# Kernel tuning notes

Measured on AMD Instinct MI355X. Metric: run time of the kernel, lower is better.

The kernel has to match this reference:

```python
import jax, jax.numpy as jnp
import numpy as np

N = 50000      # nodes
E = 600000     # edges (before self-loops)
F_IN = 128     # input features
H = 128        # hidden width
C = 64         # classes
NEG_SLOPE = 0.2


def setup_inputs() -> dict:
    key = jax.random.key(0)
    ks = jax.random.split(key, 16)
    x = jax.random.normal(ks[0], (N, F_IN), dtype=jnp.float32)
    edge_index = jax.random.randint(ks[1], (2, E), 0, N, dtype=jnp.int32)
    dims = [(F_IN, H), (H, H), (H, C)]
    inp = {"x": x, "edge_index": edge_index}
    for l, (din, dout) in enumerate(dims):
        kw, ka, kb = jax.random.split(ks[2 + l], 3)
        scale = 1.0 / np.sqrt(din)
        inp[f"W{l}"] = jax.random.normal(kw, (din, dout), dtype=jnp.float32) * scale
        inp[f"a_src{l}"] = jax.random.normal(ka, (dout,), dtype=jnp.float32) * 0.1
        inp[f"a_dst{l}"] = jax.random.normal(kb, (dout,), dtype=jnp.float32) * 0.1
        inp[f"b{l}"] = jnp.zeros((dout,), dtype=jnp.float32)
    return inp


def gat_conv(x, src, dst, W, a_s, a_d, b):
    n = x.shape[0]
    h = x @ W                                   # [n, dout]
    alpha = jax.nn.leaky_relu((h @ a_s)[src] + (h @ a_d)[dst], NEG_SLOPE)  # [e]
    # segment softmax over destination-node neighborhoods
    m = jax.ops.segment_max(alpha, dst, num_segments=n)
    ex = jnp.exp(alpha - m[dst])
    denom = jax.ops.segment_sum(ex, dst, num_segments=n)
    coef = ex / denom[dst]                      # [e]
    out = jax.ops.segment_sum(h[src] * coef[:, None], dst, num_segments=n)
    return out + b


def reference(x, edge_index, W0, a_src0, a_dst0, b0, W1, a_src1, a_dst1, b1, W2, a_src2, a_dst2, b2):
    n = x.shape[0]
    loops = jnp.arange(n, dtype=edge_index.dtype)   # add_self_loops=True (PyG default)
    src = jnp.concatenate([edge_index[0], loops])
    dst = jnp.concatenate([edge_index[1], loops])
    h = gat_conv(x, src, dst, W0, a_src0, a_dst0, b0)
    h = h * jax.nn.sigmoid(h)                        # SiLU between layers
    h = gat_conv(h, src, dst, W1, a_src1, a_dst1, b1)
    h = h * jax.nn.sigmoid(h)
    h = gat_conv(h, src, dst, W2, a_src2, a_dst2, b2)
    return jax.nn.log_softmax(h, axis=1)
```

## Files before the change

### kernel.cpp

```cpp
#include <hip/hip_runtime.h>
#include <math.h>

#define NEG_SLOPE 0.2f
constexpr int BS_SCAN = 1024;

typedef __attribute__((ext_vector_type(8))) short bfrag;
typedef __attribute__((ext_vector_type(4))) float f32x4;

__device__ __forceinline__ float lrelu(float x) { return x > 0.f ? x : NEG_SLOPE * x; }

__device__ __forceinline__ unsigned short f2bf(float f) {
    union { float f; unsigned u; } v; v.f = f;
    unsigned r = v.u + 0x7fffu + ((v.u >> 16) & 1u);
    return (unsigned short)(r >> 16);
}
__device__ __forceinline__ float bf2f_lo(unsigned p) { union { unsigned u; float f; } v; v.u = p << 16; return v.f; }
__device__ __forceinline__ float bf2f_hi(unsigned p) { union { unsigned u; float f; } v; v.u = p & 0xffff0000u; return v.f; }

__device__ __forceinline__ void wswz_body(const float* __restrict__ W, unsigned short* __restrict__ out,
                                          int DOUT, int tid) {
    int lane = tid & 63;
    int g = tid >> 6;
    int NT = DOUT >> 4;
    int tile = g % NT, kstep = g / NT;
    int q = lane >> 4, c = lane & 15;
    int n_ = tile * 16 + c;
    unsigned short v[8];
#pragma unroll
    for (int j = 0; j < 8; ++j) {
        int k = kstep * 32 + q * 8 + j;
        v[j] = f2bf(W[k * DOUT + n_]);
    }
    uint4 o;
    o.x = (unsigned)v[0] | ((unsigned)v[1] << 16);
    o.y = (unsigned)v[2] | ((unsigned)v[3] << 16);
    o.z = (unsigned)v[4] | ((unsigned)v[5] << 16);
    o.w = (unsigned)v[6] | ((unsigned)v[7] << 16);
    *(uint4*)(out + (size_t)tid * 8) = o;
}

__global__ __launch_bounds__(256) void swz_kernel(
    const float* __restrict__ W0, const float* __restrict__ W1, const float* __restrict__ W2,
    unsigned short* __restrict__ wz0, unsigned short* __restrict__ wz1, unsigned short* __restrict__ wz2)
{
    int wb = blockIdx.x;
    if (wb < 8)       wswz_body(W0, wz0, 128, wb * 256 + threadIdx.x);
    else if (wb < 16) wswz_body(W1, wz1, 128, (wb - 8) * 256 + threadIdx.x);
    else {
        int tid = (wb - 16) * 256 + threadIdx.x;
        if (tid < 1024) wswz_body(W2, wz2, 64, tid);
    }
}

__global__ __launch_bounds__(1024) void scan1_kernel(const int* __restrict__ counts,
                                                     int* __restrict__ excl,
                                                     int* __restrict__ totals, int n) {
    __shared__ int sm[BS_SCAN];
    int tid = threadIdx.x;
    int i = blockIdx.x * BS_SCAN + tid;
    int v = (i < n) ? counts[i] : 0;
    int val = v;
    sm[tid] = val;
    for (int off = 1; off < BS_SCAN; off <<= 1) {
        __syncthreads();
        int t = (tid >= off) ? sm[tid - off] : 0;
        __syncthreads();
        val += t; sm[tid] = val;
    }
    if (i < n) excl[i] = val - v;
    if (tid == BS_SCAN - 1) totals[blockIdx.x] = val;
}

__global__ __launch_bounds__(1024) void scan23_kernel(int* __restrict__ row_ptr,
                                                      const int* __restrict__ totals,
                                                      int n, int E, int nb) {
    __shared__ int s_off;
    int tid = threadIdx.x;
    if (tid < 64) {
        int v = (tid < blockIdx.x && tid < nb) ? totals[tid] : 0;
#pragma unroll
        for (int off = 32; off; off >>= 1) v += __shfl_xor(v, off);
        if (tid == 0) s_off = v;
    }
    __syncthreads();
    int off = s_off;
    int i = blockIdx.x * BS_SCAN + tid;
    if (i < n) row_ptr[i] += off;
    if (i == 0) row_ptr[n] = E;
}

template<int DOUT, bool ABF>
__device__ __forceinline__ void gemm_body(
    int bid, const void* __restrict__ Xv, const unsigned short* __restrict__ Wswz,
    const float* __restrict__ avs, const float* __restrict__ avd,
    unsigned* __restrict__ Hout, float* __restrict__ as_out, float* __restrict__ ad_out,
    int n, float* __restrict__ smemw)
{
    constexpr int NT = DOUT / 16;
    constexpr int NCH = NT / 4;
    int lane = threadIdx.x & 63;
    int w = threadIdx.x >> 6;
    int q = lane >> 4, c = lane & 15;
    int rowbase = bid * 64 + w * 16;
    int arow = rowbase + c;

    f32x4 acc[NT];
#pragma unroll
    for (int t = 0; t < NT; ++t) acc[t] = (f32x4){0.f, 0.f, 0.f, 0.f};

#pragma unroll
    for (int ks = 0; ks < 4; ++ks) {
        bfrag a = (bfrag)0;
        int k0 = ks * 32 + q * 8;
        if (ABF) {
            if (arow < n) a = *(const bfrag*)((const unsigned short*)Xv + (size_t)arow * 128 + k0);
        } else {
            if (arow < n) {
                const float* xp = (const float*)Xv + (size_t)arow * 128 + k0;
                float4 x0 = *(const float4*)xp, x1 = *(const float4*)(xp + 4);
                a[0] = (short)f2bf(x0.x); a[1] = (short)f2bf(x0.y);
                a[2] = (short)f2bf(x0.z); a[3] = (short)f2bf(x0.w);
                a[4] = (short)f2bf(x1.x); a[5] = (short)f2bf(x1.y);
                a[6] = (short)f2bf(x1.z); a[7] = (short)f2bf(x1.w);
            }
        }
#pragma unroll
        for (int t = 0; t < NT; ++t) {
            bfrag b = *(const bfrag*)(Wswz + ((size_t)(ks * NT + t) * 64 + lane) * 8);
            acc[t] = __builtin_amdgcn_mfma_f32_16x16x32_bf16(a, b, acc[t], 0, 0, 0);
        }
    }

    float* sm = smemw + w * (16 * 68);
    int dr = lane >> 2;
    int c0 = (lane & 3) * 16;
    float s = 0.f, d = 0.f;

#pragma unroll
    for (int ch = 0; ch < NCH; ++ch) {
        if (ch) {
            asm volatile("s_waitcnt lgkmcnt(0)" ::: "memory");
            __builtin_amdgcn_wave_barrier();
        }
#pragma unroll
        for (int t = 0; t < 4; ++t)
#pragma unroll
            for (int r = 0; r < 4; ++r)
                sm[(q * 4 + r) * 68 + t * 16 + c] = acc[ch * 4 + t][r];
        __builtin_amdgcn_wave_barrier();

#pragma unroll
        for (int it = 0; it < 4; ++it) {
            int r = it * 4 + q;
            int grow = rowbase + r;
            float4 v = *(const float4*)(sm + r * 68 + c * 4);
            uint2 o;
            o.x = (unsigned)f2bf(v.x) | ((unsigned)f2bf(v.y) << 16);
            o.y = (unsigned)f2bf(v.z) | ((unsigned)f2bf(v.w) << 16);
            if (grow < n) *(uint2*)(Hout + (size_t)grow * (DOUT / 2) + ch * 32 + c * 2) = o;
        }
#pragma unroll
        for (int j = 0; j < 16; j += 4) {
            float4 hv = *(const float4*)(sm + dr * 68 + c0 + j);
            float4 av = *(const float4*)(avs + ch * 64 + c0 + j);
            float4 dv = *(const float4*)(avd + ch * 64 + c0 + j);
            s += hv.x * av.x + hv.y * av.y + hv.z * av.z + hv.w * av.w;
            d += hv.x * dv.x + hv.y * dv.y + hv.z * dv.z + hv.w * dv.w;
        }
    }

    s += __shfl_down(s, 2); s += __shfl_down(s, 1);
    d += __shfl_down(d, 2); d += __shfl_down(d, 1);
    int grow = rowbase + dr;
    if ((lane & 3) == 0 && grow < n) { as_out[grow] = s; ad_out[grow] = d; }
}

__global__ __launch_bounds__(256) void fused0_kernel(
    const int* __restrict__ dstv, int* __restrict__ counts, int* __restrict__ rank, int E, int cb,
    const float* __restrict__ X, const unsigned short* __restrict__ wz0,
    const float* __restrict__ avs, const float* __restrict__ avd,
    unsigned* __restrict__ Hout, float* __restrict__ as_out, float* __restrict__ ad_out, int n)
{
    __shared__ float smem[4 * 16 * 68];
    int b = blockIdx.x;
    if (b < cb) {
        int blockbase = b * 4096 + (int)threadIdx.x * 4;
#pragma unroll
        for (int j = 0; j < 4; ++j) {
            int e0 = blockbase + j * 1024;
            if (e0 + 3 < E) {
                int4 d4 = *(const int4*)(dstv + e0);
                int4 r4;
                r4.x = atomicAdd(&counts[d4.x], 1);
                r4.y = atomicAdd(&counts[d4.y], 1);
                r4.z = atomicAdd(&counts[d4.z], 1);
                r4.w = atomicAdd(&counts[d4.w], 1);
                *(int4*)(rank + e0) = r4;
            } else {
#pragma unroll
                for (int k = 0; k < 4; ++k) {
                    int e = e0 + k;
                    if (e < E) rank[e] = atomicAdd(&counts[dstv[e]], 1);
                }
            }
        }
        return;
    }
    gemm_body<128, false>(b - cb, X, wz0, avs, avd, Hout, as_out, ad_out, n, smem);
}

template<int DOUT>
__global__ __launch_bounds__(256) void gemm_kernel(
    const unsigned* __restrict__ Xb, const unsigned short* __restrict__ Wswz,
    const float* __restrict__ avs, const float* __restrict__ avd,
    unsigned* __restrict__ Hout, float* __restrict__ as_out, float* __restrict__ ad_out, int n)
{
    __shared__ float smem[4 * 16 * 68];
    gemm_body<DOUT, true>(blockIdx.x, Xb, Wswz, avs, avd, Hout, as_out, ad_out, n, smem);
}

__global__ __launch_bounds__(256) void scatter_kernel(
    const int* __restrict__ ei, const int* __restrict__ rank,
    const int* __restrict__ row_ptr, unsigned short* __restrict__ col, int E)
{
    int blockbase = blockIdx.x * 2048 + (int)threadIdx.x * 4;
#pragma unroll
    for (int j = 0; j < 2; ++j) {
        int e0 = blockbase + j * 1024;
        if (e0 + 3 < E) {
            int4 s4 = *(const int4*)(ei + e0);
            int4 d4 = *(const int4*)(ei + E + e0);
            int4 r4 = *(const int4*)(rank + e0);
            col[row_ptr[d4.x] + r4.x] = (unsigned short)s4.x;
            col[row_ptr[d4.y] + r4.y] = (unsigned short)s4.y;
            col[row_ptr[d4.z] + r4.z] = (unsigned short)s4.z;
            col[row_ptr[d4.w] + r4.w] = (unsigned short)s4.w;
        } else {
#pragma unroll
            for (int k = 0; k < 4; ++k) {
                int e = e0 + k;
                if (e < E) col[row_ptr[ei[E + e]] + rank[e]] = (unsigned short)ei[e];
            }
        }
    }
}

__global__ __launch_bounds__(256) void agg128_kernel(
    const unsigned* __restrict__ Hb, const float* __restrict__ as_v,
    const float* __restrict__ ad_v, const float* __restrict__ bias,
    const int* __restrict__ row_ptr, const unsigned short* __restrict__ col,
    unsigned* __restrict__ outb, int n)
{
    int lane = threadIdx.x & 63;
    int node = blockIdx.x * 4 + (threadIdx.x >> 6);
    if (node >= n) return;
    int g = lane >> 4, i = lane & 15;
    int beg = row_ptr[node], end = row_ptr[node + 1];
    float adv = ad_v[node];
    float c_self = __expf(fminf(lrelu(as_v[node] + adv), 60.f));

    uint4 hs = *(const uint4*)(Hb + (size_t)node * 64 + i * 4);
    float cs0 = (g == 0) ? c_self : 0.f;
    float acc[8];
    acc[0] = cs0 * bf2f_lo(hs.x); acc[1] = cs0 * bf2f_hi(hs.x);
    acc[2] = cs0 * bf2f_lo(hs.y); acc[3] = cs0 * bf2f_hi(hs.y);
    acc[4] = cs0 * bf2f_lo(hs.z); acc[5] = cs0 * bf2f_hi(hs.z);
    acc[6] = cs0 * bf2f_lo(hs.w); acc[7] = cs0 * bf2f_hi(hs.w);
    float dsum = (lane == 0) ? c_self : 0.f;

    for (int cb = beg; cb < end; cb += 64) {
        int idx = cb + lane;
        int sreg = 0; float creg = 0.f;
        if (idx < end) {
            sreg = col[idx];
            creg = __expf(fminf(lrelu(as_v[sreg] + adv), 60.f));
        }
        dsum += creg;
        int cnt = end - cb; if (cnt > 64) cnt = 64;
        for (int k = 0; k < cnt; k += 8) {
            int kk0 = k + g, kk1 = k + g + 4;
            int s0 = __shfl(sreg, kk0);
            int s1 = __shfl(sreg, kk1);
            float c0 = __shfl(creg, kk0);
            float c1 = __shfl(creg, kk1);
            uint4 h0 = *(const uint4*)(Hb + (size_t)s0 * 64 + i * 4);
            uint4 h1 = *(const uint4*)(Hb + (size_t)s1 * 64 + i * 4);
            acc[0] += c0 * bf2f_lo(h0.x); acc[1] += c0 * bf2f_hi(h0.x);
            acc[2] += c0 * bf2f_lo(h0.y); acc[3] += c0 * bf2f_hi(h0.y);
            acc[4] += c0 * bf2f_lo(h0.z); acc[5] += c0 * bf2f_hi(h0.z);
            acc[6] += c0 * bf2f_lo(h0.w); acc[7] += c0 * bf2f_hi(h0.w);
            acc[0] += c1 * bf2f_lo(h1.x); acc[1] += c1 * bf2f_hi(h1.x);
            acc[2] += c1 * bf2f_lo(h1.y); acc[3] += c1 * bf2f_hi(h1.y);
            acc[4] += c1 * bf2f_lo(h1.z); acc[5] += c1 * bf2f_hi(h1.z);
            acc[6] += c1 * bf2f_lo(h1.w); acc[7] += c1 * bf2f_hi(h1.w);
        }
    }

#pragma unroll
    for (int off = 32; off; off >>= 1) dsum += __shfl_xor(dsum, off);
    float inv = 1.f / dsum;
#pragma unroll
    for (int j = 0; j < 8; ++j) { acc[j] += __shfl_xor(acc[j], 16); acc[j] += __shfl_xor(acc[j], 32); }

    if (g == 0) {
        float4 b0v = *(const float4*)(bias + i * 8);
        float4 b1v = *(const float4*)(bias + i * 8 + 4);
        float v0 = acc[0] * inv + b0v.x, v1 = acc[1] * inv + b0v.y;
        float v2 = acc[2] * inv + b0v.z, v3 = acc[3] * inv + b0v.w;
        float v4 = acc[4] * inv + b1v.x, v5 = acc[5] * inv + b1v.y;
        float v6 = acc[6] * inv + b1v.z, v7 = acc[7] * inv + b1v.w;
        v0 /= (1.f + __expf(-v0)); v1 /= (1.f + __expf(-v1));
        v2 /= (1.f + __expf(-v2)); v3 /= (1.f + __expf(-v3));
        v4 /= (1.f + __expf(-v4)); v5 /= (1.f + __expf(-v5));
        v6 /= (1.f + __expf(-v6)); v7 /= (1.f + __expf(-v7));
        uint4 o;
        o.x = (unsigned)f2bf(v0) | ((unsigned)f2bf(v1) << 16);
        o.y = (unsigned)f2bf(v2) | ((unsigned)f2bf(v3) << 16);
        o.z = (unsigned)f2bf(v4) | ((unsigned)f2bf(v5) << 16);
        o.w = (unsigned)f2bf(v6) | ((unsigned)f2bf(v7) << 16);
        *(uint4*)(outb + (size_t)node * 64 + i * 4) = o;
    }
}

__global__ __launch_bounds__(256) void agg64_kernel(
    const unsigned* __restrict__ Hb, const float* __restrict__ as_v,
    const float* __restrict__ ad_v, const float* __restrict__ bias,
    const int* __restrict__ row_ptr, const unsigned short* __restrict__ col,
    float* __restrict__ out, int n)
{
    int lane = threadIdx.x & 63;
    int node = blockIdx.x * 4 + (threadIdx.x >> 6);
    if (node >= n) return;
    int g = lane >> 4, i = lane & 15;
    int beg = row_ptr[node], end = row_ptr[node + 1];
    float adv = ad_v[node];
    float c_self = __expf(fminf(lrelu(as_v[node] + adv), 60.f));

    uint2 hs = *(const uint2*)(Hb + (size_t)node * 32 + i * 2);
    float cs0 = (g == 0) ? c_self : 0.f;
    float acc[4];
    acc[0] = cs0 * bf2f_lo(hs.x); acc[1] = cs0 * bf2f_hi(hs.x);
    acc[2] = cs0 * bf2f_lo(hs.y); acc[3] = cs0 * bf2f_hi(hs.y);
    float dsum = (lane == 0) ? c_self : 0.f;

    for (int cb = beg; cb < end; cb += 64) {
        int idx = cb + lane;
        int sreg = 0; float creg = 0.f;
        if (idx < end) {
            sreg = col[idx];
            creg = __expf(fminf(lrelu(as_v[sreg] + adv), 60.f));
        }
        dsum += creg;
        int cnt = end - cb; if (cnt > 64) cnt = 64;
        for (int k = 0; k < cnt; k += 8) {
            int kk0 = k + g, kk1 = k + g + 4;
            int s0 = __shfl(sreg, kk0);
            int s1 = __shfl(sreg, kk1);
            float c0 = __shfl(creg, kk0);
            float c1 = __shfl(creg, kk1);
            uint2 h0 = *(const uint2*)(Hb + (size_t)s0 * 32 + i * 2);
            uint2 h1 = *(const uint2*)(Hb + (size_t)s1 * 32 + i * 2);
            acc[0] += c0 * bf2f_lo(h0.x); acc[1] += c0 * bf2f_hi(h0.x);
            acc[2] += c0 * bf2f_lo(h0.y); acc[3] += c0 * bf2f_hi(h0.y);
            acc[0] += c1 * bf2f_lo(h1.x); acc[1] += c1 * bf2f_hi(h1.x);
            acc[2] += c1 * bf2f_lo(h1.y); acc[3] += c1 * bf2f_hi(h1.y);
        }
    }

#pragma unroll
    for (int off = 32; off; off >>= 1) dsum += __shfl_xor(dsum, off);
    float inv = 1.f / dsum;
#pragma unroll
    for (int j = 0; j < 4; ++j) { acc[j] += __shfl_xor(acc[j], 16); acc[j] += __shfl_xor(acc[j], 32); }

    float4 bv = *(const float4*)(bias + i * 4);
    float v0 = acc[0] * inv + bv.x, v1 = acc[1] * inv + bv.y;
    float v2 = acc[2] * inv + bv.z, v3 = acc[3] * inv + bv.w;
    float mx = fmaxf(fmaxf(v0, v1), fmaxf(v2, v3));
#pragma unroll
    for (int off = 8; off; off >>= 1) mx = fmaxf(mx, __shfl_xor(mx, off));
    float sum = __expf(v0 - mx) + __expf(v1 - mx) + __expf(v2 - mx) + __expf(v3 - mx);
#pragma unroll
    for (int off = 8; off; off >>= 1) sum += __shfl_xor(sum, off);
    float ls = mx + logf(sum);
    if (g == 0) {
        float4 o = make_float4(v0 - ls, v1 - ls, v2 - ls, v3 - ls);
        *(float4*)(out + (size_t)node * 64 + i * 4) = o;
    }
}

extern "C" void kernel_launch(void* const* d_in, const int* in_sizes, int n_in,
                              void* d_out, int out_size, void* d_ws, size_t ws_size,
                              hipStream_t stream) {
    const float* x   = (const float*)d_in[0];
    const int*   ei  = (const int*)d_in[1];
    const float* W0  = (const float*)d_in[2];
    const float* as0 = (const float*)d_in[3];
    const float* ad0 = (const float*)d_in[4];
    const float* b0  = (const float*)d_in[5];
    const float* W1  = (const float*)d_in[6];
    const float* as1 = (const float*)d_in[7];
    const float* ad1 = (const float*)d_in[8];
    const float* b1  = (const float*)d_in[9];
    const float* W2  = (const float*)d_in[10];
    const float* as2 = (const float*)d_in[11];
    const float* ad2 = (const float*)d_in[12];
    const float* b2  = (const float*)d_in[13];

    int n = in_sizes[0] / 128;
    int E = in_sizes[1] / 2;
    const int* dstv = ei + E;

    char* wsp = (char*)d_ws;
    auto alloc = [&](size_t bytes) {
        char* p = wsp;
        wsp += (bytes + 255) & ~(size_t)255;
        return p;
    };
    int*   counts  = (int*)alloc((size_t)n * 4);
    int*   row_ptr = (int*)alloc((size_t)(n + 1) * 4);
    int*   rank    = (int*)alloc((size_t)E * 4);
    int*   totals  = (int*)alloc(256 * 4);
    unsigned short* col = (unsigned short*)alloc((size_t)E * 2);
    unsigned short* wz0 = (unsigned short*)alloc(128 * 128 * 2);
    unsigned short* wz1 = (unsigned short*)alloc(128 * 128 * 2);
    unsigned short* wz2 = (unsigned short*)alloc(128 * 64 * 2);
    unsigned* hb0  = (unsigned*)alloc((size_t)n * 64 * 4);
    unsigned* hb1  = (unsigned*)alloc((size_t)n * 64 * 4);
    unsigned* hf   = (unsigned*)alloc((size_t)n * 32 * 4);
    unsigned* xb   = (unsigned*)alloc((size_t)n * 64 * 4);
    float*    asbA = (float*)alloc((size_t)n * 4);
    float*    adbA = (float*)alloc((size_t)n * 4);
    float*    asbB = (float*)alloc((size_t)n * 4);
    float*    adbB = (float*)alloc((size_t)n * 4);

    (void)hipMemsetAsync(counts, 0, (size_t)n * 4, stream);
    int cbc   = (E + 4095) / 4096;
    int cbs   = (E + 2047) / 2048;
    int gemmb = (n + 63) / 64;
    int nodeb = (n + 3) / 4;
    int nb = (n + BS_SCAN - 1) / BS_SCAN;

    swz_kernel<<<20, 256, 0, stream>>>(W0, W1, W2, wz0, wz1, wz2);
    fused0_kernel<<<cbc + gemmb, 256, 0, stream>>>(dstv, counts, rank, E, cbc,
                                                   x, wz0, as0, ad0, hb0, asbA, adbA, n);
    scan1_kernel<<<nb, BS_SCAN, 0, stream>>>(counts, row_ptr, totals, n);
    scan23_kernel<<<nb, BS_SCAN, 0, stream>>>(row_ptr, totals, n, E, nb);
    scatter_kernel<<<cbs, 256, 0, stream>>>(ei, rank, row_ptr, col, E);
    agg128_kernel<<<nodeb, 256, 0, stream>>>(hb0, asbA, adbA, b0, row_ptr, col, xb, n);
    gemm_kernel<128><<<gemmb, 256, 0, stream>>>(xb, wz1, as1, ad1, hb1, asbB, adbB, n);
    agg128_kernel<<<nodeb, 256, 0, stream>>>(hb1, asbB, adbB, b1, row_ptr, col, xb, n);
    gemm_kernel<64><<<gemmb, 256, 0, stream>>>(xb, wz2, as2, ad2, hf, asbA, adbA, n);
    agg64_kernel<<<nodeb, 256, 0, stream>>>(hf, asbA, adbA, b2, row_ptr, col, (float*)d_out, n);
}
```

Measured before the change: 261.8 us.

## Build CSR with cursor atomics instead of per-edge rank, fold memset, unroll gathers

The counting pass no longer stores a per-edge rank array. Instead the scan writes a per-node cursor, and the scatter kernel claims slots with atomicAdd on that cursor, batching 16 edges per thread. The counts memset is folded into the weight-swizzle kernel, which removes one launch. The aggregation inner loops now gather four neighbor rows per iteration instead of two, for more memory-level parallelism. Neighbor order within each CSR row becomes nondeterministic, which can change float summation order slightly, and the scatter now pays for atomics.

```diff
diff --git a/kernel.cpp b/kernel.cpp
--- a/kernel.cpp
+++ b/kernel.cpp
@@ -41,14 +41,18 @@
 
 __global__ __launch_bounds__(256) void swz_kernel(
     const float* __restrict__ W0, const float* __restrict__ W1, const float* __restrict__ W2,
-    unsigned short* __restrict__ wz0, unsigned short* __restrict__ wz1, unsigned short* __restrict__ wz2)
+    unsigned short* __restrict__ wz0, unsigned short* __restrict__ wz1, unsigned short* __restrict__ wz2,
+    int* __restrict__ counts, int n)
 {
     int wb = blockIdx.x;
     if (wb < 8)       wswz_body(W0, wz0, 128, wb * 256 + threadIdx.x);
     else if (wb < 16) wswz_body(W1, wz1, 128, (wb - 8) * 256 + threadIdx.x);
-    else {
+    else if (wb < 20) {
         int tid = (wb - 16) * 256 + threadIdx.x;
         if (tid < 1024) wswz_body(W2, wz2, 64, tid);
+    } else {
+        int i = (wb - 20) * 256 + (int)threadIdx.x;
+        if (i < n) counts[i] = 0;
     }
 }
 
@@ -73,7 +77,7 @@
 
 __global__ __launch_bounds__(1024) void scan23_kernel(int* __restrict__ row_ptr,
                                                       const int* __restrict__ totals,
-                                                      int n, int E, int nb) {
+                                                      int* __restrict__ cursor, int n, int E, int nb) {
     __shared__ int s_off;
     int tid = threadIdx.x;
     if (tid < 64) {
@@ -85,7 +89,11 @@
     __syncthreads();
     int off = s_off;
     int i = blockIdx.x * BS_SCAN + tid;
-    if (i < n) row_ptr[i] += off;
+    if (i < n) {
+        int rp = row_ptr[i] + off;
+        row_ptr[i] = rp;
+        cursor[i] = rp;
+    }
     if (i == 0) row_ptr[n] = E;
 }
 
@@ -176,7 +184,7 @@
 }
 
 __global__ __launch_bounds__(256) void fused0_kernel(
-    const int* __restrict__ dstv, int* __restrict__ counts, int* __restrict__ rank, int E, int cb,
+    const int* __restrict__ dstv, int* __restrict__ counts, int E, int cb,
     const float* __restrict__ X, const unsigned short* __restrict__ wz0,
     const float* __restrict__ avs, const float* __restrict__ avd,
     unsigned* __restrict__ Hout, float* __restrict__ as_out, float* __restrict__ ad_out, int n)
@@ -188,19 +196,17 @@
 #pragma unroll
         for (int j = 0; j < 4; ++j) {
             int e0 = blockbase + j * 1024;
-            if (e0 + 3 < E) {
+            if (((E & 3) == 0) && e0 + 3 < E) {
                 int4 d4 = *(const int4*)(dstv + e0);
-                int4 r4;
-                r4.x = atomicAdd(&counts[d4.x], 1);
-                r4.y = atomicAdd(&counts[d4.y], 1);
-                r4.z = atomicAdd(&counts[d4.z], 1);
-                r4.w = atomicAdd(&counts[d4.w], 1);
-                *(int4*)(rank + e0) = r4;
+                atomicAdd(&counts[d4.x], 1);
+                atomicAdd(&counts[d4.y], 1);
+                atomicAdd(&counts[d4.z], 1);
+                atomicAdd(&counts[d4.w], 1);
             } else {
 #pragma unroll
                 for (int k = 0; k < 4; ++k) {
                     int e = e0 + k;
-                    if (e < E) rank[e] = atomicAdd(&counts[dstv[e]], 1);
+                    if (e < E) atomicAdd(&counts[dstv[e]], 1);
                 }
             }
         }
@@ -220,26 +226,35 @@
 }
 
 __global__ __launch_bounds__(256) void scatter_kernel(
-    const int* __restrict__ ei, const int* __restrict__ rank,
-    const int* __restrict__ row_ptr, unsigned short* __restrict__ col, int E)
-{
-    int blockbase = blockIdx.x * 2048 + (int)threadIdx.x * 4;
-#pragma unroll
-    for (int j = 0; j < 2; ++j) {
-        int e0 = blockbase + j * 1024;
-        if (e0 + 3 < E) {
+    const int* __restrict__ ei, int* __restrict__ cursor,
+    unsigned short* __restrict__ col, int E)
+{
+    int blockbase = blockIdx.x * 4096 + (int)threadIdx.x * 4;
+    if (((E & 3) == 0) && (blockIdx.x + 1) * 4096 <= E) {
+        int dd[16], ss[16], pp[16];
+#pragma unroll
+        for (int j = 0; j < 4; ++j) {
+            int e0 = blockbase + j * 1024;
+            int4 d4 = *(const int4*)(ei + E + e0);
             int4 s4 = *(const int4*)(ei + e0);
-            int4 d4 = *(const int4*)(ei + E + e0);
-            int4 r4 = *(const int4*)(rank + e0);
-            col[row_ptr[d4.x] + r4.x] = (unsigned short)s4.x;
-            col[row_ptr[d4.y] + r4.y] = (unsigned short)s4.y;
-            col[row_ptr[d4.z] + r4.z] = (unsigned short)s4.z;
-            col[row_ptr[d4.w] + r4.w] = (unsigned short)s4.w;
-        } else {
+            dd[j * 4 + 0] = d4.x; dd[j * 4 + 1] = d4.y; dd[j * 4 + 2] = d4.z; dd[j * 4 + 3] = d4.w;
+            ss[j * 4 + 0] = s4.x; ss[j * 4 + 1] = s4.y; ss[j * 4 + 2] = s4.z; ss[j * 4 + 3] = s4.w;
+        }
+#pragma unroll
+        for (int i = 0; i < 16; ++i) pp[i] = atomicAdd(&cursor[dd[i]], 1);
+#pragma unroll
+        for (int i = 0; i < 16; ++i) col[pp[i]] = (unsigned short)ss[i];
+    } else {
+#pragma unroll
+        for (int j = 0; j < 4; ++j) {
+            int e0 = blockbase + j * 1024;
 #pragma unroll
             for (int k = 0; k < 4; ++k) {
                 int e = e0 + k;
-                if (e < E) col[row_ptr[ei[E + e]] + rank[e]] = (unsigned short)ei[e];
+                if (e < E) {
+                    int pos = atomicAdd(&cursor[ei[E + e]], 1);
+                    col[pos] = (unsigned short)ei[e];
+                }
             }
         }
     }
@@ -277,14 +292,20 @@
         }
         dsum += creg;
         int cnt = end - cb; if (cnt > 64) cnt = 64;
-        for (int k = 0; k < cnt; k += 8) {
-            int kk0 = k + g, kk1 = k + g + 4;
+        for (int k = 0; k < cnt; k += 16) {
+            int kk0 = k + g, kk1 = k + g + 4, kk2 = k + g + 8, kk3 = k + g + 12;
             int s0 = __shfl(sreg, kk0);
             int s1 = __shfl(sreg, kk1);
+            int s2 = __shfl(sreg, kk2);
+            int s3 = __shfl(sreg, kk3);
             float c0 = __shfl(creg, kk0);
             float c1 = __shfl(creg, kk1);
+            float c2 = __shfl(creg, kk2);
+            float c3 = __shfl(creg, kk3);
             uint4 h0 = *(const uint4*)(Hb + (size_t)s0 * 64 + i * 4);
             uint4 h1 = *(const uint4*)(Hb + (size_t)s1 * 64 + i * 4);
+            uint4 h2 = *(const uint4*)(Hb + (size_t)s2 * 64 + i * 4);
+            uint4 h3 = *(const uint4*)(Hb + (size_t)s3 * 64 + i * 4);
             acc[0] += c0 * bf2f_lo(h0.x); acc[1] += c0 * bf2f_hi(h0.x);
             acc[2] += c0 * bf2f_lo(h0.y); acc[3] += c0 * bf2f_hi(h0.y);
             acc[4] += c0 * bf2f_lo(h0.z); acc[5] += c0 * bf2f_hi(h0.z);
@@ -293,6 +314,14 @@
             acc[2] += c1 * bf2f_lo(h1.y); acc[3] += c1 * bf2f_hi(h1.y);
             acc[4] += c1 * bf2f_lo(h1.z); acc[5] += c1 * bf2f_hi(h1.z);
             acc[6] += c1 * bf2f_lo(h1.w); acc[7] += c1 * bf2f_hi(h1.w);
+            acc[0] += c2 * bf2f_lo(h2.x); acc[1] += c2 * bf2f_hi(h2.x);
+            acc[2] += c2 * bf2f_lo(h2.y); acc[3] += c2 * bf2f_hi(h2.y);
+            acc[4] += c2 * bf2f_lo(h2.z); acc[5] += c2 * bf2f_hi(h2.z);
+            acc[6] += c2 * bf2f_lo(h2.w); acc[7] += c2 * bf2f_hi(h2.w);
+            acc[0] += c3 * bf2f_lo(h3.x); acc[1] += c3 * bf2f_hi(h3.x);
+            acc[2] += c3 * bf2f_lo(h3.y); acc[3] += c3 * bf2f_hi(h3.y);
+            acc[4] += c3 * bf2f_lo(h3.z); acc[5] += c3 * bf2f_hi(h3.z);
+            acc[6] += c3 * bf2f_lo(h3.w); acc[7] += c3 * bf2f_hi(h3.w);
         }
     }
 
@@ -352,18 +381,28 @@
         }
         dsum += creg;
         int cnt = end - cb; if (cnt > 64) cnt = 64;
-        for (int k = 0; k < cnt; k += 8) {
-            int kk0 = k + g, kk1 = k + g + 4;
+        for (int k = 0; k < cnt; k += 16) {
+            int kk0 = k + g, kk1 = k + g + 4, kk2 = k + g + 8, kk3 = k + g + 12;
             int s0 = __shfl(sreg, kk0);
             int s1 = __shfl(sreg, kk1);
+            int s2 = __shfl(sreg, kk2);
+            int s3 = __shfl(sreg, kk3);
             float c0 = __shfl(creg, kk0);
             float c1 = __shfl(creg, kk1);
+            float c2 = __shfl(creg, kk2);
+            float c3 = __shfl(creg, kk3);
             uint2 h0 = *(const uint2*)(Hb + (size_t)s0 * 32 + i * 2);
             uint2 h1 = *(const uint2*)(Hb + (size_t)s1 * 32 + i * 2);
+            uint2 h2 = *(const uint2*)(Hb + (size_t)s2 * 32 + i * 2);
+            uint2 h3 = *(const uint2*)(Hb + (size_t)s3 * 32 + i * 2);
             acc[0] += c0 * bf2f_lo(h0.x); acc[1] += c0 * bf2f_hi(h0.x);
             acc[2] += c0 * bf2f_lo(h0.y); acc[3] += c0 * bf2f_hi(h0.y);
             acc[0] += c1 * bf2f_lo(h1.x); acc[1] += c1 * bf2f_hi(h1.x);
             acc[2] += c1 * bf2f_lo(h1.y); acc[3] += c1 * bf2f_hi(h1.y);
+            acc[0] += c2 * bf2f_lo(h2.x); acc[1] += c2 * bf2f_hi(h2.x);
+            acc[2] += c2 * bf2f_lo(h2.y); acc[3] += c2 * bf2f_hi(h2.y);
+            acc[0] += c3 * bf2f_lo(h3.x); acc[1] += c3 * bf2f_hi(h3.x);
+            acc[2] += c3 * bf2f_lo(h3.y); acc[3] += c3 * bf2f_hi(h3.y);
         }
     }
 
@@ -419,7 +458,7 @@
     };
     int*   counts  = (int*)alloc((size_t)n * 4);
     int*   row_ptr = (int*)alloc((size_t)(n + 1) * 4);
-    int*   rank    = (int*)alloc((size_t)E * 4);
+    int*   cursor  = (int*)alloc((size_t)n * 4);
     int*   totals  = (int*)alloc(256 * 4);
     unsigned short* col = (unsigned short*)alloc((size_t)E * 2);
     unsigned short* wz0 = (unsigned short*)alloc(128 * 128 * 2);
@@ -434,19 +473,18 @@
     float*    asbB = (float*)alloc((size_t)n * 4);
     float*    adbB = (float*)alloc((size_t)n * 4);
 
-    (void)hipMemsetAsync(counts, 0, (size_t)n * 4, stream);
     int cbc   = (E + 4095) / 4096;
-    int cbs   = (E + 2047) / 2048;
     int gemmb = (n + 63) / 64;
     int nodeb = (n + 3) / 4;
     int nb = (n + BS_SCAN - 1) / BS_SCAN;
-
-    swz_kernel<<<20, 256, 0, stream>>>(W0, W1, W2, wz0, wz1, wz2);
-    fused0_kernel<<<cbc + gemmb, 256, 0, stream>>>(dstv, counts, rank, E, cbc,
+    int zb = (n + 255) / 256;
+
+    swz_kernel<<<20 + zb, 256, 0, stream>>>(W0, W1, W2, wz0, wz1, wz2, counts, n);
+    fused0_kernel<<<cbc + gemmb, 256, 0, stream>>>(dstv, counts, E, cbc,
                                                    x, wz0, as0, ad0, hb0, asbA, adbA, n);
     scan1_kernel<<<nb, BS_SCAN, 0, stream>>>(counts, row_ptr, totals, n);
-    scan23_kernel<<<nb, BS_SCAN, 0, stream>>>(row_ptr, totals, n, E, nb);
-    scatter_kernel<<<cbs, 256, 0, stream>>>(ei, rank, row_ptr, col, E);
+    scan23_kernel<<<nb, BS_SCAN, 0, stream>>>(row_ptr, totals, cursor, n, E, nb);
+    scatter_kernel<<<cbc, 256, 0, stream>>>(ei, cursor, col, E);
     agg128_kernel<<<nodeb, 256, 0, stream>>>(hb0, asbA, adbA, b0, row_ptr, col, xb, n);
     gemm_kernel<128><<<gemmb, 256, 0, stream>>>(xb, wz1, as1, ad1, hb1, asbB, adbB, n);
     agg128_kernel<<<nodeb, 256, 0, stream>>>(hb1, asbB, adbB, b1, row_ptr, col, xb, n);
```

Result: slower. 273.8 us (+4.6%).

## Replace global atomic degree counting with per-block LDS byte histograms

Applied to the files above, without the earlier changes.

Edge-to-destination counting moves from global atomics into per-block shared-memory histograms of 8-bit counters packed four per word. Each block writes its histogram out, a new column-scan kernel forms per-block offsets and per-node counts, and the scatter kernel rebuilds each edge's slot from the block offset plus its local byte rank. Ranks shrink from int to byte. The cost is two large per-block histogram arrays, a serial scan over blocks, and a much larger shared-memory allocation that the fused GEMM blocks also carry. The packed byte counters assume every node's in-degree stays below 256, which holds only for low-degree graphs.

```diff
diff --git a/kernel.cpp b/kernel.cpp
--- a/kernel.cpp
+++ b/kernel.cpp
@@ -176,37 +176,104 @@
 }
 
 __global__ __launch_bounds__(256) void fused0_kernel(
-    const int* __restrict__ dstv, int* __restrict__ counts, int* __restrict__ rank, int E, int cb,
+    const int* __restrict__ dstv, unsigned* __restrict__ hist32, unsigned char* __restrict__ rank8,
+    int E, int hb, int nw,
     const float* __restrict__ X, const unsigned short* __restrict__ wz0,
     const float* __restrict__ avs, const float* __restrict__ avd,
     unsigned* __restrict__ Hout, float* __restrict__ as_out, float* __restrict__ ad_out, int n)
 {
-    __shared__ float smem[4 * 16 * 68];
+    __shared__ unsigned sbuf[12544];
     int b = blockIdx.x;
-    if (b < cb) {
-        int blockbase = b * 4096 + (int)threadIdx.x * 4;
+    if (b < hb) {
+        int tid = threadIdx.x;
+        for (int i = tid; i < nw; i += 256) sbuf[i] = 0u;
+        __syncthreads();
+        int base = b * 4096;
 #pragma unroll
         for (int j = 0; j < 4; ++j) {
-            int e0 = blockbase + j * 1024;
+            int e0 = base + j * 1024 + tid * 4;
             if (e0 + 3 < E) {
                 int4 d4 = *(const int4*)(dstv + e0);
-                int4 r4;
-                r4.x = atomicAdd(&counts[d4.x], 1);
-                r4.y = atomicAdd(&counts[d4.y], 1);
-                r4.z = atomicAdd(&counts[d4.z], 1);
-                r4.w = atomicAdd(&counts[d4.w], 1);
-                *(int4*)(rank + e0) = r4;
+                unsigned r0, r1, r2, r3;
+                { int sh = (d4.x & 3) * 8; r0 = (atomicAdd(&sbuf[d4.x >> 2], 1u << sh) >> sh) & 0xffu; }
+                { int sh = (d4.y & 3) * 8; r1 = (atomicAdd(&sbuf[d4.y >> 2], 1u << sh) >> sh) & 0xffu; }
+                { int sh = (d4.z & 3) * 8; r2 = (atomicAdd(&sbuf[d4.z >> 2], 1u << sh) >> sh) & 0xffu; }
+                { int sh = (d4.w & 3) * 8; r3 = (atomicAdd(&sbuf[d4.w >> 2], 1u << sh) >> sh) & 0xffu; }
+                *(unsigned*)(rank8 + e0) = r0 | (r1 << 8) | (r2 << 16) | (r3 << 24);
             } else {
-#pragma unroll
                 for (int k = 0; k < 4; ++k) {
                     int e = e0 + k;
-                    if (e < E) rank[e] = atomicAdd(&counts[dstv[e]], 1);
+                    if (e < E) {
+                        int d = dstv[e];
+                        int sh = (d & 3) * 8;
+                        rank8[e] = (unsigned char)((atomicAdd(&sbuf[d >> 2], 1u << sh) >> sh) & 0xffu);
+                    }
                 }
             }
         }
+        __syncthreads();
+        unsigned* hrow = hist32 + (size_t)b * nw;
+        for (int i = tid; i < nw; i += 256) hrow[i] = sbuf[i];
         return;
     }
-    gemm_body<128, false>(b - cb, X, wz0, avs, avd, Hout, as_out, ad_out, n, smem);
+    gemm_body<128, false>(b - hb, X, wz0, avs, avd, Hout, as_out, ad_out, n, (float*)sbuf);
+}
+
+__global__ __launch_bounds__(256) void colscan_kernel(
+    const unsigned* __restrict__ hist32, unsigned* __restrict__ off32,
+    int* __restrict__ counts, int hb, int nw, int n)
+{
+    int iw = blockIdx.x * 256 + (int)threadIdx.x;
+    if (iw >= nw) return;
+    unsigned run = 0;
+    for (int b = 0; b < hb; ++b) {
+        size_t idx = (size_t)b * nw + iw;
+        unsigned c = hist32[idx];
+        off32[idx] = run;
+        run += c;
+    }
+    int i0 = iw * 4;
+    int4 cv;
+    cv.x = (int)(run & 0xffu); cv.y = (int)((run >> 8) & 0xffu);
+    cv.z = (int)((run >> 16) & 0xffu); cv.w = (int)((run >> 24) & 0xffu);
+    if (i0 + 3 < n) *(int4*)(counts + i0) = cv;
+    else {
+        if (i0 < n)     counts[i0] = cv.x;
+        if (i0 + 1 < n) counts[i0 + 1] = cv.y;
+        if (i0 + 2 < n) counts[i0 + 2] = cv.z;
+        if (i0 + 3 < n) counts[i0 + 3] = cv.w;
+    }
+}
+
+__global__ __launch_bounds__(256) void scatter_kernel(
+    const int* __restrict__ ei, const unsigned char* __restrict__ rank8,
+    const unsigned* __restrict__ off32, const int* __restrict__ row_ptr,
+    unsigned short* __restrict__ col, int E, int nw)
+{
+    int e0 = (blockIdx.x * 256 + (int)threadIdx.x) * 4;
+    if (e0 + 3 < E) {
+        int4 s4 = *(const int4*)(ei + e0);
+        int4 d4 = *(const int4*)(ei + E + e0);
+        unsigned r4 = *(const unsigned*)(rank8 + e0);
+        size_t bb = (size_t)(e0 >> 12) * nw;
+        unsigned o0 = (off32[bb + (d4.x >> 2)] >> ((d4.x & 3) * 8)) & 0xffu;
+        unsigned o1 = (off32[bb + (d4.y >> 2)] >> ((d4.y & 3) * 8)) & 0xffu;
+        unsigned o2 = (off32[bb + (d4.z >> 2)] >> ((d4.z & 3) * 8)) & 0xffu;
+        unsigned o3 = (off32[bb + (d4.w >> 2)] >> ((d4.w & 3) * 8)) & 0xffu;
+        col[row_ptr[d4.x] + (int)o0 + (int)(r4 & 0xffu)]         = (unsigned short)s4.x;
+        col[row_ptr[d4.y] + (int)o1 + (int)((r4 >> 8) & 0xffu)]  = (unsigned short)s4.y;
+        col[row_ptr[d4.z] + (int)o2 + (int)((r4 >> 16) & 0xffu)] = (unsigned short)s4.z;
+        col[row_ptr[d4.w] + (int)o3 + (int)((r4 >> 24) & 0xffu)] = (unsigned short)s4.w;
+    } else {
+        for (int k = 0; k < 4; ++k) {
+            int e = e0 + k;
+            if (e < E) {
+                int d = ei[E + e];
+                unsigned o = (off32[(size_t)(e >> 12) * nw + (d >> 2)] >> ((d & 3) * 8)) & 0xffu;
+                col[row_ptr[d] + (int)o + (int)rank8[e]] = (unsigned short)ei[e];
+            }
+        }
+    }
 }
 
 template<int DOUT>
@@ -217,32 +284,6 @@
 {
     __shared__ float smem[4 * 16 * 68];
     gemm_body<DOUT, true>(blockIdx.x, Xb, Wswz, avs, avd, Hout, as_out, ad_out, n, smem);
-}
-
-__global__ __launch_bounds__(256) void scatter_kernel(
-    const int* __restrict__ ei, const int* __restrict__ rank,
-    const int* __restrict__ row_ptr, unsigned short* __restrict__ col, int E)
-{
-    int blockbase = blockIdx.x * 2048 + (int)threadIdx.x * 4;
-#pragma unroll
-    for (int j = 0; j < 2; ++j) {
-        int e0 = blockbase + j * 1024;
-        if (e0 + 3 < E) {
-            int4 s4 = *(const int4*)(ei + e0);
-            int4 d4 = *(const int4*)(ei + E + e0);
-            int4 r4 = *(const int4*)(rank + e0);
-            col[row_ptr[d4.x] + r4.x] = (unsigned short)s4.x;
-            col[row_ptr[d4.y] + r4.y] = (unsigned short)s4.y;
-            col[row_ptr[d4.z] + r4.z] = (unsigned short)s4.z;
-            col[row_ptr[d4.w] + r4.w] = (unsigned short)s4.w;
-        } else {
-#pragma unroll
-            for (int k = 0; k < 4; ++k) {
-                int e = e0 + k;
-                if (e < E) col[row_ptr[ei[E + e]] + rank[e]] = (unsigned short)ei[e];
-            }
-        }
-    }
 }
 
 __global__ __launch_bounds__(256) void agg128_kernel(
@@ -411,6 +452,9 @@
     int E = in_sizes[1] / 2;
     const int* dstv = ei + E;
 
+    int hb = (E + 4095) >> 12;
+    int nw = (n + 3) >> 2;
+
     char* wsp = (char*)d_ws;
     auto alloc = [&](size_t bytes) {
         char* p = wsp;
@@ -419,8 +463,10 @@
     };
     int*   counts  = (int*)alloc((size_t)n * 4);
     int*   row_ptr = (int*)alloc((size_t)(n + 1) * 4);
-    int*   rank    = (int*)alloc((size_t)E * 4);
     int*   totals  = (int*)alloc(256 * 4);
+    unsigned* hist32 = (unsigned*)alloc((size_t)hb * nw * 4);
+    unsigned* off32  = (unsigned*)alloc((size_t)hb * nw * 4);
+    unsigned char* rank8 = (unsigned char*)alloc((size_t)E);
     unsigned short* col = (unsigned short*)alloc((size_t)E * 2);
     unsigned short* wz0 = (unsigned short*)alloc(128 * 128 * 2);
     unsigned short* wz1 = (unsigned short*)alloc(128 * 128 * 2);
@@ -434,19 +480,19 @@
     float*    asbB = (float*)alloc((size_t)n * 4);
     float*    adbB = (float*)alloc((size_t)n * 4);
 
-    (void)hipMemsetAsync(counts, 0, (size_t)n * 4, stream);
-    int cbc   = (E + 4095) / 4096;
-    int cbs   = (E + 2047) / 2048;
     int gemmb = (n + 63) / 64;
     int nodeb = (n + 3) / 4;
-    int nb = (n + BS_SCAN - 1) / BS_SCAN;
+    int nb  = (n + BS_SCAN - 1) / BS_SCAN;
+    int cwb = (nw + 255) / 256;
+    int scb = (E + 1023) / 1024;
 
     swz_kernel<<<20, 256, 0, stream>>>(W0, W1, W2, wz0, wz1, wz2);
-    fused0_kernel<<<cbc + gemmb, 256, 0, stream>>>(dstv, counts, rank, E, cbc,
-                                                   x, wz0, as0, ad0, hb0, asbA, adbA, n);
+    fused0_kernel<<<hb + gemmb, 256, 0, stream>>>(dstv, hist32, rank8, E, hb, nw,
+                                                  x, wz0, as0, ad0, hb0, asbA, adbA, n);
+    colscan_kernel<<<cwb, 256, 0, stream>>>(hist32, off32, counts, hb, nw, n);
     scan1_kernel<<<nb, BS_SCAN, 0, stream>>>(counts, row_ptr, totals, n);
     scan23_kernel<<<nb, BS_SCAN, 0, stream>>>(row_ptr, totals, n, E, nb);
-    scatter_kernel<<<cbs, 256, 0, stream>>>(ei, rank, row_ptr, col, E);
+    scatter_kernel<<<scb, 256, 0, stream>>>(ei, rank8, off32, row_ptr, col, E, nw);
     agg128_kernel<<<nodeb, 256, 0, stream>>>(hb0, asbA, adbA, b0, row_ptr, col, xb, n);
     gemm_kernel<128><<<gemmb, 256, 0, stream>>>(xb, wz1, as1, ad1, hb1, asbB, adbB, n);
     agg128_kernel<<<nodeb, 256, 0, stream>>>(hb1, asbB, adbB, b1, row_ptr, col, xb, n);
```

Result: slower. 282.4 us (+7.8%).

## Map one 16-lane group per node in aggregation and fold counts zeroing into swizzle

Applied to the files above, without the earlier changes.

The aggregation kernels now assign each 16-lane quarter-wavefront its own destination node instead of one full wavefront per node. This removes the cross-group shuffle reductions and the idle lanes during the epilogue, and unrolls the neighbour gather by four. Separately, the memset of the degree counts is folded into the weight-swizzle kernel as extra blocks, saving one launch. The risk is more divergence between groups within a wavefront when node degrees differ, since each group loops over its own edges.

```diff
diff --git a/kernel.cpp b/kernel.cpp
--- a/kernel.cpp
+++ b/kernel.cpp
@@ -41,14 +41,18 @@
 
 __global__ __launch_bounds__(256) void swz_kernel(
     const float* __restrict__ W0, const float* __restrict__ W1, const float* __restrict__ W2,
-    unsigned short* __restrict__ wz0, unsigned short* __restrict__ wz1, unsigned short* __restrict__ wz2)
+    unsigned short* __restrict__ wz0, unsigned short* __restrict__ wz1, unsigned short* __restrict__ wz2,
+    int* __restrict__ counts, int n)
 {
     int wb = blockIdx.x;
     if (wb < 8)       wswz_body(W0, wz0, 128, wb * 256 + threadIdx.x);
     else if (wb < 16) wswz_body(W1, wz1, 128, (wb - 8) * 256 + threadIdx.x);
-    else {
+    else if (wb < 20) {
         int tid = (wb - 16) * 256 + threadIdx.x;
         if (tid < 1024) wswz_body(W2, wz2, 64, tid);
+    } else {
+        int i = (wb - 20) * 256 + (int)threadIdx.x;
+        if (i < n) counts[i] = 0;
     }
 }
 
@@ -252,39 +256,44 @@
     unsigned* __restrict__ outb, int n)
 {
     int lane = threadIdx.x & 63;
-    int node = blockIdx.x * 4 + (threadIdx.x >> 6);
+    int g = lane >> 4, i = lane & 15;
+    int node = blockIdx.x * 16 + (threadIdx.x >> 6) * 4 + g;
     if (node >= n) return;
-    int g = lane >> 4, i = lane & 15;
     int beg = row_ptr[node], end = row_ptr[node + 1];
     float adv = ad_v[node];
     float c_self = __expf(fminf(lrelu(as_v[node] + adv), 60.f));
 
     uint4 hs = *(const uint4*)(Hb + (size_t)node * 64 + i * 4);
-    float cs0 = (g == 0) ? c_self : 0.f;
     float acc[8];
-    acc[0] = cs0 * bf2f_lo(hs.x); acc[1] = cs0 * bf2f_hi(hs.x);
-    acc[2] = cs0 * bf2f_lo(hs.y); acc[3] = cs0 * bf2f_hi(hs.y);
-    acc[4] = cs0 * bf2f_lo(hs.z); acc[5] = cs0 * bf2f_hi(hs.z);
-    acc[6] = cs0 * bf2f_lo(hs.w); acc[7] = cs0 * bf2f_hi(hs.w);
-    float dsum = (lane == 0) ? c_self : 0.f;
-
-    for (int cb = beg; cb < end; cb += 64) {
-        int idx = cb + lane;
+    acc[0] = c_self * bf2f_lo(hs.x); acc[1] = c_self * bf2f_hi(hs.x);
+    acc[2] = c_self * bf2f_lo(hs.y); acc[3] = c_self * bf2f_hi(hs.y);
+    acc[4] = c_self * bf2f_lo(hs.z); acc[5] = c_self * bf2f_hi(hs.z);
+    acc[6] = c_self * bf2f_lo(hs.w); acc[7] = c_self * bf2f_hi(hs.w);
+    float dsum = (i == 0) ? c_self : 0.f;
+    int lanebase = g * 16;
+
+    for (int cb = beg; cb < end; cb += 16) {
+        int idx = cb + i;
         int sreg = 0; float creg = 0.f;
         if (idx < end) {
             sreg = col[idx];
             creg = __expf(fminf(lrelu(as_v[sreg] + adv), 60.f));
         }
         dsum += creg;
-        int cnt = end - cb; if (cnt > 64) cnt = 64;
-        for (int k = 0; k < cnt; k += 8) {
-            int kk0 = k + g, kk1 = k + g + 4;
-            int s0 = __shfl(sreg, kk0);
-            int s1 = __shfl(sreg, kk1);
-            float c0 = __shfl(creg, kk0);
-            float c1 = __shfl(creg, kk1);
+        int cnt = end - cb; if (cnt > 16) cnt = 16;
+        for (int k = 0; k < cnt; k += 4) {
+            int s0 = __shfl(sreg, lanebase + k);
+            int s1 = __shfl(sreg, lanebase + k + 1);
+            int s2 = __shfl(sreg, lanebase + k + 2);
+            int s3 = __shfl(sreg, lanebase + k + 3);
+            float c0 = __shfl(creg, lanebase + k);
+            float c1 = __shfl(creg, lanebase + k + 1);
+            float c2 = __shfl(creg, lanebase + k + 2);
+            float c3 = __shfl(creg, lanebase + k + 3);
             uint4 h0 = *(const uint4*)(Hb + (size_t)s0 * 64 + i * 4);
             uint4 h1 = *(const uint4*)(Hb + (size_t)s1 * 64 + i * 4);
+            uint4 h2 = *(const uint4*)(Hb + (size_t)s2 * 64 + i * 4);
+            uint4 h3 = *(const uint4*)(Hb + (size_t)s3 * 64 + i * 4);
             acc[0] += c0 * bf2f_lo(h0.x); acc[1] += c0 * bf2f_hi(h0.x);
             acc[2] += c0 * bf2f_lo(h0.y); acc[3] += c0 * bf2f_hi(h0.y);
             acc[4] += c0 * bf2f_lo(h0.z); acc[5] += c0 * bf2f_hi(h0.z);
@@ -293,33 +302,37 @@
             acc[2] += c1 * bf2f_lo(h1.y); acc[3] += c1 * bf2f_hi(h1.y);
             acc[4] += c1 * bf2f_lo(h1.z); acc[5] += c1 * bf2f_hi(h1.z);
             acc[6] += c1 * bf2f_lo(h1.w); acc[7] += c1 * bf2f_hi(h1.w);
-        }
-    }
-
-#pragma unroll
-    for (int off = 32; off; off >>= 1) dsum += __shfl_xor(dsum, off);
+            acc[0] += c2 * bf2f_lo(h2.x); acc[1] += c2 * bf2f_hi(h2.x);
+            acc[2] += c2 * bf2f_lo(h2.y); acc[3] += c2 * bf2f_hi(h2.y);
+            acc[4] += c2 * bf2f_lo(h2.z); acc[5] += c2 * bf2f_hi(h2.z);
+            acc[6] += c2 * bf2f_lo(h2.w); acc[7] += c2 * bf2f_hi(h2.w);
+            acc[0] += c3 * bf2f_lo(h3.x); acc[1] += c3 * bf2f_hi(h3.x);
+            acc[2] += c3 * bf2f_lo(h3.y); acc[3] += c3 * bf2f_hi(h3.y);
+            acc[4] += c3 * bf2f_lo(h3.z); acc[5] += c3 * bf2f_hi(h3.z);
+            acc[6] += c3 * bf2f_lo(h3.w); acc[7] += c3 * bf2f_hi(h3.w);
+        }
+    }
+
+#pragma unroll
+    for (int off = 8; off; off >>= 1) dsum += __shfl_xor(dsum, off);
     float inv = 1.f / dsum;
-#pragma unroll
-    for (int j = 0; j < 8; ++j) { acc[j] += __shfl_xor(acc[j], 16); acc[j] += __shfl_xor(acc[j], 32); }
-
-    if (g == 0) {
-        float4 b0v = *(const float4*)(bias + i * 8);
-        float4 b1v = *(const float4*)(bias + i * 8 + 4);
-        float v0 = acc[0] * inv + b0v.x, v1 = acc[1] * inv + b0v.y;
-        float v2 = acc[2] * inv + b0v.z, v3 = acc[3] * inv + b0v.w;
-        float v4 = acc[4] * inv + b1v.x, v5 = acc[5] * inv + b1v.y;
-        float v6 = acc[6] * inv + b1v.z, v7 = acc[7] * inv + b1v.w;
-        v0 /= (1.f + __expf(-v0)); v1 /= (1.f + __expf(-v1));
-        v2 /= (1.f + __expf(-v2)); v3 /= (1.f + __expf(-v3));
-        v4 /= (1.f + __expf(-v4)); v5 /= (1.f + __expf(-v5));
-        v6 /= (1.f + __expf(-v6)); v7 /= (1.f + __expf(-v7));
-        uint4 o;
-        o.x = (unsigned)f2bf(v0) | ((unsigned)f2bf(v1) << 16);
-        o.y = (unsigned)f2bf(v2) | ((unsigned)f2bf(v3) << 16);
-        o.z = (unsigned)f2bf(v4) | ((unsigned)f2bf(v5) << 16);
-        o.w = (unsigned)f2bf(v6) | ((unsigned)f2bf(v7) << 16);
-        *(uint4*)(outb + (size_t)node * 64 + i * 4) = o;
-    }
+
+    float4 b0v = *(const float4*)(bias + i * 8);
+    float4 b1v = *(const float4*)(bias + i * 8 + 4);
+    float v0 = acc[0] * inv + b0v.x, v1 = acc[1] * inv + b0v.y;
+    float v2 = acc[2] * inv + b0v.z, v3 = acc[3] * inv + b0v.w;
+    float v4 = acc[4] * inv + b1v.x, v5 = acc[5] * inv + b1v.y;
+    float v6 = acc[6] * inv + b1v.z, v7 = acc[7] * inv + b1v.w;
+    v0 /= (1.f + __expf(-v0)); v1 /= (1.f + __expf(-v1));
+    v2 /= (1.f + __expf(-v2)); v3 /= (1.f + __expf(-v3));
+    v4 /= (1.f + __expf(-v4)); v5 /= (1.f + __expf(-v5));
+    v6 /= (1.f + __expf(-v6)); v7 /= (1.f + __expf(-v7));
+    uint4 o;
+    o.x = (unsigned)f2bf(v0) | ((unsigned)f2bf(v1) << 16);
+    o.y = (unsigned)f2bf(v2) | ((unsigned)f2bf(v3) << 16);
+    o.z = (unsigned)f2bf(v4) | ((unsigned)f2bf(v5) << 16);
+    o.w = (unsigned)f2bf(v6) | ((unsigned)f2bf(v7) << 16);
+    *(uint4*)(outb + (size_t)node * 64 + i * 4) = o;
 }
 
 __global__ __launch_bounds__(256) void agg64_kernel(
@@ -329,49 +342,56 @@
     float* __restrict__ out, int n)
 {
     int lane = threadIdx.x & 63;
-    int node = blockIdx.x * 4 + (threadIdx.x >> 6);
+    int g = lane >> 4, i = lane & 15;
+    int node = blockIdx.x * 16 + (threadIdx.x >> 6) * 4 + g;
     if (node >= n) return;
-    int g = lane >> 4, i = lane & 15;
     int beg = row_ptr[node], end = row_ptr[node + 1];
     float adv = ad_v[node];
     float c_self = __expf(fminf(lrelu(as_v[node] + adv), 60.f));
 
     uint2 hs = *(const uint2*)(Hb + (size_t)node * 32 + i * 2);
-    float cs0 = (g == 0) ? c_self : 0.f;
     float acc[4];
-    acc[0] = cs0 * bf2f_lo(hs.x); acc[1] = cs0 * bf2f_hi(hs.x);
-    acc[2] = cs0 * bf2f_lo(hs.y); acc[3] = cs0 * bf2f_hi(hs.y);
-    float dsum = (lane == 0) ? c_self : 0.f;
-
-    for (int cb = beg; cb < end; cb += 64) {
-        int idx = cb + lane;
+    acc[0] = c_self * bf2f_lo(hs.x); acc[1] = c_self * bf2f_hi(hs.x);
+    acc[2] = c_self * bf2f_lo(hs.y); acc[3] = c_self * bf2f_hi(hs.y);
+    float dsum = (i == 0) ? c_self : 0.f;
+    int lanebase = g * 16;
+
+    for (int cb = beg; cb < end; cb += 16) {
+        int idx = cb + i;
         int sreg = 0; float creg = 0.f;
         if (idx < end) {
             sreg = col[idx];
             creg = __expf(fminf(lrelu(as_v[sreg] + adv), 60.f));
         }
         dsum += creg;
-        int cnt = end - cb; if (cnt > 64) cnt = 64;
-        for (int k = 0; k < cnt; k += 8) {
-            int kk0 = k + g, kk1 = k + g + 4;
-            int s0 = __shfl(sreg, kk0);
-            int s1 = __shfl(sreg, kk1);
-            float c0 = __shfl(creg, kk0);
-            float c1 = __shfl(creg, kk1);
+        int cnt = end - cb; if (cnt > 16) cnt = 16;
+        for (int k = 0; k < cnt; k += 4) {
+            int s0 = __shfl(sreg, lanebase + k);
+            int s1 = __shfl(sreg, lanebase + k + 1);
+            int s2 = __shfl(sreg, lanebase + k + 2);
+            int s3 = __shfl(sreg, lanebase + k + 3);
+            float c0 = __shfl(creg, lanebase + k);
+            float c1 = __shfl(creg, lanebase + k + 1);
+            float c2 = __shfl(creg, lanebase + k + 2);
+            float c3 = __shfl(creg, lanebase + k + 3);
             uint2 h0 = *(const uint2*)(Hb + (size_t)s0 * 32 + i * 2);
             uint2 h1 = *(const uint2*)(Hb + (size_t)s1 * 32 + i * 2);
+            uint2 h2 = *(const uint2*)(Hb + (size_t)s2 * 32 + i * 2);
+            uint2 h3 = *(const uint2*)(Hb + (size_t)s3 * 32 + i * 2);
             acc[0] += c0 * bf2f_lo(h0.x); acc[1] += c0 * bf2f_hi(h0.x);
             acc[2] += c0 * bf2f_lo(h0.y); acc[3] += c0 * bf2f_hi(h0.y);
             acc[0] += c1 * bf2f_lo(h1.x); acc[1] += c1 * bf2f_hi(h1.x);
             acc[2] += c1 * bf2f_lo(h1.y); acc[3] += c1 * bf2f_hi(h1.y);
-        }
-    }
-
-#pragma unroll
-    for (int off = 32; off; off >>= 1) dsum += __shfl_xor(dsum, off);
+            acc[0] += c2 * bf2f_lo(h2.x); acc[1] += c2 * bf2f_hi(h2.x);
+            acc[2] += c2 * bf2f_lo(h2.y); acc[3] += c2 * bf2f_hi(h2.y);
+            acc[0] += c3 * bf2f_lo(h3.x); acc[1] += c3 * bf2f_hi(h3.x);
+            acc[2] += c3 * bf2f_lo(h3.y); acc[3] += c3 * bf2f_hi(h3.y);
+        }
+    }
+
+#pragma unroll
+    for (int off = 8; off; off >>= 1) dsum += __shfl_xor(dsum, off);
     float inv = 1.f / dsum;
-#pragma unroll
-    for (int j = 0; j < 4; ++j) { acc[j] += __shfl_xor(acc[j], 16); acc[j] += __shfl_xor(acc[j], 32); }
 
     float4 bv = *(const float4*)(bias + i * 4);
     float v0 = acc[0] * inv + bv.x, v1 = acc[1] * inv + bv.y;
@@ -383,10 +403,8 @@
 #pragma unroll
     for (int off = 8; off; off >>= 1) sum += __shfl_xor(sum, off);
     float ls = mx + logf(sum);
-    if (g == 0) {
-        float4 o = make_float4(v0 - ls, v1 - ls, v2 - ls, v3 - ls);
-        *(float4*)(out + (size_t)node * 64 + i * 4) = o;
-    }
+    float4 o = make_float4(v0 - ls, v1 - ls, v2 - ls, v3 - ls);
+    *(float4*)(out + (size_t)node * 64 + i * 4) = o;
 }
 
 extern "C" void kernel_launch(void* const* d_in, const int* in_sizes, int n_in,
@@ -434,14 +452,14 @@
     float*    asbB = (float*)alloc((size_t)n * 4);
     float*    adbB = (float*)alloc((size_t)n * 4);
 
-    (void)hipMemsetAsync(counts, 0, (size_t)n * 4, stream);
     int cbc   = (E + 4095) / 4096;
     int cbs   = (E + 2047) / 2048;
     int gemmb = (n + 63) / 64;
-    int nodeb = (n + 3) / 4;
+    int nodeb = (n + 15) / 16;
     int nb = (n + BS_SCAN - 1) / BS_SCAN;
-
-    swz_kernel<<<20, 256, 0, stream>>>(W0, W1, W2, wz0, wz1, wz2);
+    int zb = (n + 255) / 256;
+
+    swz_kernel<<<20 + zb, 256, 0, stream>>>(W0, W1, W2, wz0, wz1, wz2, counts, n);
     fused0_kernel<<<cbc + gemmb, 256, 0, stream>>>(dstv, counts, rank, E, cbc,
                                                    x, wz0, as0, ad0, hb0, asbA, adbA, n);
     scan1_kernel<<<nb, BS_SCAN, 0, stream>>>(counts, row_ptr, totals, n);
```

Measured after the change: 233.0 us. 1.12x faster.
